# Kernel optimization log

Hardware: AMD Instinct MI355X
Metric: run time of the kernel (lower is better)

## Reference

```python
import jax, jax.numpy as jnp
import numpy as np

N_SRC = 50000
N_DST = 50000
IN_F = 128
OUT_F = 128
N_TYPES = 3
FANOUT = 10
LN_EPS = 1e-12


def setup_inputs() -> dict:
    key = jax.random.key(0)
    ks = jax.random.split(key, 12)
    s_in = 1.0 / np.sqrt(IN_F)
    return {
        "feature": jax.random.normal(ks[0], (N_SRC, IN_F), jnp.float32),
        "neighbor_idx": jax.random.randint(ks[1], (N_TYPES, N_DST, FANOUT), 0, N_SRC),
        "W_ih": jax.random.normal(ks[2], (N_TYPES, 4 * IN_F, IN_F), jnp.float32) * s_in,
        "W_hh": jax.random.normal(ks[3], (N_TYPES, 4 * IN_F, IN_F), jnp.float32) * s_in,
        "b_ih": jax.random.normal(ks[4], (N_TYPES, 4 * IN_F), jnp.float32) * s_in,
        "b_hh": jax.random.normal(ks[5], (N_TYPES, 4 * IN_F), jnp.float32) * s_in,
        "fc_self_w": jax.random.normal(ks[6], (N_TYPES, OUT_F, IN_F), jnp.float32) * s_in,
        "fc_neigh_w": jax.random.normal(ks[7], (N_TYPES, OUT_F, IN_F), jnp.float32) * s_in,
        "sage_bias": jnp.zeros((N_TYPES, OUT_F), jnp.float32),
        "ln_w": jnp.ones((N_TYPES, OUT_F), jnp.float32),
        "ln_b": jnp.zeros((N_TYPES, OUT_F), jnp.float32),
    }


def _lstm_last_hidden(seq, W_ih, W_hh, b_ih, b_hh):
    # seq: [N, F, H_in]; single-layer LSTM, hidden size = input size (DGL SAGEConv lstm reducer).
    N = seq.shape[0]
    H = W_hh.shape[1]
    b = b_ih + b_hh

    def step(carry, x):
        h, c = carry
        gates = x @ W_ih.T + h @ W_hh.T + b  # [N, 4H]
        i, f, g, o = jnp.split(gates, 4, axis=-1)  # torch gate order i,f,g,o
        c = jax.nn.sigmoid(f) * c + jax.nn.sigmoid(i) * jnp.tanh(g)
        h = jax.nn.sigmoid(o) * jnp.tanh(c)
        return (h, c), None

    init = (jnp.zeros((N, H), seq.dtype), jnp.zeros((N, H), seq.dtype))
    (h_n, _), _ = jax.lax.scan(step, init, jnp.swapaxes(seq, 0, 1))
    return h_n  # [N, H]


def _layernorm(x, w, b):
    u = jnp.mean(x, axis=-1, keepdims=True)
    s = jnp.mean((x - u) ** 2, axis=-1, keepdims=True)
    return w * ((x - u) / jnp.sqrt(s + LN_EPS)) + b


def reference(feature, neighbor_idx, W_ih, W_hh, b_ih, b_hh,
              fc_self_w, fc_neigh_w, sage_bias, ln_w, ln_b):
    outs = []
    n_types = neighbor_idx.shape[0]
    for t in range(n_types):
        neigh = feature[neighbor_idx[t]]  # [N_dst, fanout, IN_F] irregular gather
        h_neigh = _lstm_last_hidden(neigh, W_ih[t], W_hh[t], b_ih[t], b_hh[t])
        rst = feature @ fc_self_w[t].T + h_neigh @ fc_neigh_w[t].T + sage_bias[t]
        h = _layernorm(rst, ln_w[t], ln_b[t])
        h = jax.nn.elu(h)  # dropout p=0.0 -> identity
        outs.append(h)
    return jnp.stack(outs, axis=1)  # [N_dst, n_types, OUT_F]
```

## Files before the change

kernel.cpp:

```cpp
#include <hip/hip_runtime.h>
#include <hip/hip_bf16.h>

#define N_SRC_ 50000
#define N_DST_ 50000
#define INF_   128
#define OUTF_  128
#define NT_    3
#define FAN_   10
#define BM_    64

#define LOG2E_  1.4426950408889634f
#define LOG2E2_ 2.8853900817779268f

typedef __attribute__((ext_vector_type(8))) short          bf16x8;
typedef __attribute__((ext_vector_type(4))) float          f32x4;
typedef __attribute__((ext_vector_type(2))) float          f32x2;

__device__ __forceinline__ unsigned short f2bf(float f) {
  unsigned u = __float_as_uint(f);
  u = u + 0x7FFFu + ((u >> 16) & 1u);
  return (unsigned short)(u >> 16);
}
__device__ __forceinline__ float frcp(float x) { return __builtin_amdgcn_rcpf(x); }
__device__ __forceinline__ float fexp2(float x) { return __builtin_amdgcn_exp2f(x); }

__device__ __forceinline__ void gload16(const unsigned short* g, unsigned short* l) {
  __builtin_amdgcn_global_load_lds(
      (const __attribute__((address_space(1))) void*)g,
      (__attribute__((address_space(3))) void*)l, 16, 0, 0);
}

__global__ void prep_feat(const float* __restrict__ f, unsigned short* __restrict__ o, int n4) {
  int i = blockIdx.x * blockDim.x + threadIdx.x;
  if (i < n4) {
    float4 v = ((const float4*)f)[i];
    ushort4 r;
    r.x = f2bf(v.x); r.y = f2bf(v.y); r.z = f2bf(v.z); r.w = f2bf(v.w);
    ((ushort4*)o)[i] = r;
  }
}

__global__ void prep_w(const float* __restrict__ W_ih, const float* __restrict__ W_hh,
                       const float* __restrict__ b_ih, const float* __restrict__ b_hh,
                       const float* __restrict__ fcs,  const float* __restrict__ fcn,
                       unsigned short* __restrict__ Wcat, unsigned short* __restrict__ W2cat,
                       float* __restrict__ bcat) {
  int i = blockIdx.x * blockDim.x + threadIdx.x;
  if (i < NT_ * 512 * 256) {
    int t = i / (512 * 256); int rem = i % (512 * 256);
    int nr = rem >> 8; int kk = rem & 255;
    int w = nr >> 6, ct = (nr >> 4) & 3, j = nr & 15;
    int col = ct * 128 + w * 16 + j;
    float v = (kk < 128) ? W_ih[(t * 512 + col) * 128 + kk]
                         : W_hh[(t * 512 + col) * 128 + (kk - 128)];
    v *= (ct == 2) ? LOG2E2_ : LOG2E_;
    Wcat[i] = f2bf(v);
  } else {
    int i2 = i - NT_ * 512 * 256;
    if (i2 < NT_ * 128 * 256) {
      int t = i2 / (128 * 256); int rem = i2 % (128 * 256);
      int n = rem >> 8; int kk = rem & 255;
      float v = (kk < 128) ? fcs[(t * 128 + n) * 128 + kk]
                           : fcn[(t * 128 + n) * 128 + (kk - 128)];
      W2cat[i2] = f2bf(v);
    } else {
      int i3 = i2 - NT_ * 128 * 256;
      if (i3 < NT_ * 512) {
        int t = i3 / 512; int nr = i3 % 512;
        int ct = (nr >> 4) & 3;
        int col = ct * 128 + (nr >> 6) * 16 + (nr & 15);
        float s = (ct == 2) ? LOG2E2_ : LOG2E_;
        bcat[i3] = (b_ih[t * 512 + col] + b_hh[t * 512 + col]) * s;
      }
    }
  }
}

__global__ __launch_bounds__(512, 2) void sage_main(
    const unsigned short* __restrict__ feat16, const int* __restrict__ nidx,
    const unsigned short* __restrict__ Wcat, const float* __restrict__ bcat,
    const unsigned short* __restrict__ W2cat,
    const float* __restrict__ sbias, const float* __restrict__ lnw,
    const float* __restrict__ lnb, float* __restrict__ out) {
  const int t  = blockIdx.y;
  const int r0 = blockIdx.x * BM_;
  const int tid = threadIdx.x;
  const int w  = tid >> 6;
  const int l  = tid & 63;
  const int lg = l >> 4;
  const int lr = l & 15;

  __shared__ __align__(16) unsigned short lds_x[2][BM_ * INF_];
  __shared__ __align__(16) unsigned short lds_h[2][BM_ * INF_];
  __shared__ int   lds_idx[BM_ * FAN_];
  __shared__ float lds_ps[BM_ * 8];
  __shared__ float lds_pq[BM_ * 8];
  __shared__ float lds_mu[BM_];
  __shared__ float lds_ri[BM_];

  for (int i = tid; i < BM_ * FAN_; i += 512) {
    int row = i / FAN_;
    int v = 0;
    if (r0 + row < N_DST_) v = nidx[(t * N_DST_ + r0) * FAN_ + i];
    v = min(max(v, 0), N_SRC_ - 1);
    lds_idx[i] = v * INF_;
  }

  bf16x8 wfrag[4][8];
  {
    const unsigned short* wb = Wcat + (t * 512 + w * 64) * 256;
#pragma unroll
    for (int ct = 0; ct < 4; ++ct)
#pragma unroll
      for (int kk = 0; kk < 8; ++kk)
        wfrag[ct][kk] = *(const bf16x8*)(wb + (ct * 16 + lr) * 256 + kk * 32 + lg * 8);
  }
  f32x4 biasv[4];
#pragma unroll
  for (int ct = 0; ct < 4; ++ct)
#pragma unroll
    for (int j = 0; j < 4; ++j)
      biasv[ct][j] = bcat[t * 512 + w * 64 + ct * 16 + lg * 4 + j];

  float cst[16];
#pragma unroll
  for (int q = 0; q < 16; ++q) cst[q] = 0.f;

  const int grow = tid >> 4;
  const int gch  = tid & 15;
  const int gsw  = (gch ^ (grow & 7)) * 8;
  const int wb0  = (w * 4) * INF_;
  const int wb1  = (w * 4 + 32) * INF_;
  const int amask = (lr & 7) << 3;
  const int hcw   = w * 2 + (lg >> 1);
  const int hoff  = (lg & 1) << 2;

  __syncthreads();

  {
    int o0 = lds_idx[grow * FAN_];
    int o1 = lds_idx[(grow + 32) * FAN_];
    gload16(feat16 + o0 + gsw, &lds_x[0][wb0]);
    gload16(feat16 + o1 + gsw, &lds_x[0][wb1]);
  }
  __syncthreads();

#pragma unroll 1
  for (int k = 0; k < FAN_; ++k) {
    const int cb = k & 1, nb = cb ^ 1;

    if (k + 1 < FAN_) {
      int o0 = lds_idx[grow * FAN_ + k + 1];
      int o1 = lds_idx[(grow + 32) * FAN_ + k + 1];
      gload16(feat16 + o0 + gsw, &lds_x[nb][wb0]);
      gload16(feat16 + o1 + gsw, &lds_x[nb][wb1]);
    } else {
      int s0 = min(r0 + grow, N_DST_ - 1) * INF_;
      int s1 = min(r0 + grow + 32, N_DST_ - 1) * INF_;
      gload16(feat16 + s0 + gsw, &lds_x[nb][wb0]);
      gload16(feat16 + s1 + gsw, &lds_x[nb][wb1]);
    }

    const unsigned short* xb = lds_x[cb];
    const unsigned short* hb = lds_h[cb];
    unsigned short* hw = lds_h[nb];

    auto mfma_rt = [&](f32x4* acc, int rt) {
#pragma unroll
      for (int ct = 0; ct < 4; ++ct) acc[ct] = biasv[ct];
      __builtin_amdgcn_s_setprio(1);
#pragma unroll
      for (int kk = 0; kk < 8; ++kk) {
        if (kk >= 4 && k == 0) continue;
        const int rowb = (rt * 16 + lr) * INF_;
        bf16x8 b = (kk < 4)
            ? *(const bf16x8*)(xb + rowb + ((kk * 32 + lg * 8) ^ amask))
            : *(const bf16x8*)(hb + rowb + (((kk - 4) * 32 + lg * 8) ^ amask));
#pragma unroll
        for (int ct = 0; ct < 4; ++ct)
          acc[ct] = __builtin_amdgcn_mfma_f32_16x16x32_bf16(wfrag[ct][kk], b, acc[ct], 0, 0, 0);
      }
      __builtin_amdgcn_s_setprio(0);
    };

    auto gates_rt = [&](f32x4* acc, int rt) {
      float hv[4];
#pragma unroll
      for (int jp = 0; jp < 2; ++jp) {
        f32x2 gi = {acc[0][jp * 2], acc[0][jp * 2 + 1]};
        f32x2 gf = {acc[1][jp * 2], acc[1][jp * 2 + 1]};
        f32x2 gg = {acc[2][jp * 2], acc[2][jp * 2 + 1]};
        f32x2 go = {acc[3][jp * 2], acc[3][jp * 2 + 1]};
        f32x2 ei, ef, Eg, eo;
        ei[0] = fexp2(-gi[0]); ei[1] = fexp2(-gi[1]);
        ef[0] = fexp2(-gf[0]); ef[1] = fexp2(-gf[1]);
        Eg[0] = fexp2(gg[0]);  Eg[1] = fexp2(gg[1]);
        eo[0] = fexp2(-go[0]); eo[1] = fexp2(-go[1]);
        f32x2 A = ef + 1.f;
        f32x2 B = ei + 1.f;
        f32x2 E = Eg + 1.f;
        f32x2 F = Eg - 1.f;
        f32x2 cp = {cst[rt * 4 + jp * 2], cst[rt * 4 + jp * 2 + 1]};
        f32x2 BE = B * E;
        f32x2 den = A * BE;
        f32x2 r; r[0] = frcp(den[0]); r[1] = frcp(den[1]);
        f32x2 c2 = (cp * BE + F * A) * r;
        cst[rt * 4 + jp * 2]     = c2[0];
        cst[rt * 4 + jp * 2 + 1] = c2[1];
        f32x2 xc = c2 * LOG2E2_;
        f32x2 Ec; Ec[0] = fexp2(xc[0]); Ec[1] = fexp2(xc[1]);
        f32x2 G = Ec - 1.f;
        f32x2 H = (eo + 1.f) * (Ec + 1.f);
        f32x2 rr; rr[0] = frcp(H[0]); rr[1] = frcp(H[1]);
        f32x2 hvv = G * rr;
        hv[jp * 2] = hvv[0]; hv[jp * 2 + 1] = hvv[1];
      }
      unsigned p01, p23;
      asm("v_cvt_pk_bf16_f32 %0, %1, %2" : "=v"(p01) : "v"(hv[0]), "v"(hv[1]));
      asm("v_cvt_pk_bf16_f32 %0, %1, %2" : "=v"(p23) : "v"(hv[2]), "v"(hv[3]));
      const int row = rt * 16 + lr;
      const int saddr = row * INF_ + (((hcw ^ (row & 7)) << 3) + hoff);
      uint2 pk; pk.x = p01; pk.y = p23;
      *(uint2*)(hw + saddr) = pk;
    };

    f32x4 accA[4], accB[4];
    mfma_rt(accA, 0);
    mfma_rt(accB, 1);
    gates_rt(accA, 0);
    mfma_rt(accA, 2);
    gates_rt(accB, 1);
    mfma_rt(accB, 3);
    gates_rt(accA, 2);
    gates_rt(accB, 3);

    __syncthreads();
  }

  bf16x8 w2f[8];
  {
    const unsigned short* w2b = W2cat + (t * 128 + w * 16) * 256;
#pragma unroll
    for (int kk = 0; kk < 8; ++kk)
      w2f[kk] = *(const bf16x8*)(w2b + lr * 256 + kk * 32 + lg * 8);
  }
  f32x4 b2v, lwv, lbv;
#pragma unroll
  for (int j = 0; j < 4; ++j) {
    b2v[j] = sbias[t * 128 + w * 16 + lg * 4 + j];
    lwv[j] = lnw[t * 128 + w * 16 + lg * 4 + j];
    lbv[j] = lnb[t * 128 + w * 16 + lg * 4 + j];
  }

  f32x4 a2[4];
#pragma unroll
  for (int rt = 0; rt < 4; ++rt) a2[rt] = b2v;
  {
    const unsigned short* xb = lds_x[0];
    const unsigned short* hb = lds_h[0];
    __builtin_amdgcn_s_setprio(1);
#pragma unroll
    for (int kk = 0; kk < 8; ++kk) {
#pragma unroll
      for (int rt = 0; rt < 4; ++rt) {
        const int rowb = (rt * 16 + lr) * INF_;
        bf16x8 b = (kk < 4)
            ? *(const bf16x8*)(xb + rowb + ((kk * 32 + lg * 8) ^ amask))
            : *(const bf16x8*)(hb + rowb + (((kk - 4) * 32 + lg * 8) ^ amask));
        a2[rt] = __builtin_amdgcn_mfma_f32_16x16x32_bf16(w2f[kk], b, a2[rt], 0, 0, 0);
      }
    }
    __builtin_amdgcn_s_setprio(0);
  }

#pragma unroll
  for (int rt = 0; rt < 4; ++rt) {
    float s = a2[rt][0] + a2[rt][1] + a2[rt][2] + a2[rt][3];
    float q = a2[rt][0] * a2[rt][0] + a2[rt][1] * a2[rt][1]
            + a2[rt][2] * a2[rt][2] + a2[rt][3] * a2[rt][3];
    s += __shfl_xor(s, 16, 64); q += __shfl_xor(q, 16, 64);
    s += __shfl_xor(s, 32, 64); q += __shfl_xor(q, 32, 64);
    if (lg == 0) {
      int row = rt * 16 + lr;
      lds_ps[row * 8 + w] = s;
      lds_pq[row * 8 + w] = q;
    }
  }
  __syncthreads();
  if (tid < BM_) {
    float s = 0.f, q = 0.f;
#pragma unroll
    for (int wv = 0; wv < 8; ++wv) { s += lds_ps[tid * 8 + wv]; q += lds_pq[tid * 8 + wv]; }
    float mu = s * (1.f / 128.f);
    float var = q * (1.f / 128.f) - mu * mu;
    lds_mu[tid] = mu;
    lds_ri[tid] = rsqrtf(var + 1e-12f);
  }
  __syncthreads();
#pragma unroll
  for (int rt = 0; rt < 4; ++rt) {
    int row = rt * 16 + lr;
    if (r0 + row < N_DST_) {
      float mu = lds_mu[row], ri = lds_ri[row];
      float4 o;
      float y0 = (a2[rt][0] - mu) * ri * lwv[0] + lbv[0];
      float y1 = (a2[rt][1] - mu) * ri * lwv[1] + lbv[1];
      float y2 = (a2[rt][2] - mu) * ri * lwv[2] + lbv[2];
      float y3 = (a2[rt][3] - mu) * ri * lwv[3] + lbv[3];
      o.x = (y0 > 0.f) ? y0 : (fexp2(y0 * LOG2E_) - 1.f);
      o.y = (y1 > 0.f) ? y1 : (fexp2(y1 * LOG2E_) - 1.f);
      o.z = (y2 > 0.f) ? y2 : (fexp2(y2 * LOG2E_) - 1.f);
      o.w = (y3 > 0.f) ? y3 : (fexp2(y3 * LOG2E_) - 1.f);
      *(float4*)(out + (size_t)(r0 + row) * (NT_ * OUTF_) + t * OUTF_ + w * 16 + lg * 4) = o;
    }
  }
}

extern "C" void kernel_launch(void* const* d_in, const int* in_sizes, int n_in,
                              void* d_out, int out_size, void* d_ws, size_t ws_size,
                              hipStream_t stream) {
  (void)in_sizes; (void)n_in; (void)out_size; (void)ws_size;
  const float* feature = (const float*)d_in[0];
  const int*   nidx    = (const int*)d_in[1];
  const float* W_ih    = (const float*)d_in[2];
  const float* W_hh    = (const float*)d_in[3];
  const float* b_ih    = (const float*)d_in[4];
  const float* b_hh    = (const float*)d_in[5];
  const float* fcs     = (const float*)d_in[6];
  const float* fcn     = (const float*)d_in[7];
  const float* sbias   = (const float*)d_in[8];
  const float* lnw     = (const float*)d_in[9];
  const float* lnb     = (const float*)d_in[10];
  float* out = (float*)d_out;

  char* ws = (char*)d_ws;
  unsigned short* feat16 = (unsigned short*)ws;
  unsigned short* Wcat   = (unsigned short*)(ws + 12800000);
  unsigned short* W2cat  = (unsigned short*)(ws + 12800000 + 786432);
  float*          bcat   = (float*)(ws + 12800000 + 786432 + 196608);

  int n4 = N_SRC_ * INF_ / 4;
  prep_feat<<<(n4 + 255) / 256, 256, 0, stream>>>(feature, feat16, n4);
  int ptot = NT_ * 512 * 256 + NT_ * 128 * 256 + NT_ * 512;
  prep_w<<<(ptot + 255) / 256, 256, 0, stream>>>(W_ih, W_hh, b_ih, b_hh, fcs, fcn, Wcat, W2cat, bcat);

  dim3 grid((N_DST_ + BM_ - 1) / BM_, NT_);
  sage_main<<<grid, 512, 0, stream>>>(feat16, nidx, Wcat, bcat, W2cat, sbias, lnw, lnb, out);
}
```

Measured before the change: 495.4 us.

## Peel first LSTM step and interleave MFMA with gate math via sched_group_barrier

Peels the k=0 LSTM step into its own block that skips the zero-hidden-state MFMAs, and makes the steady-state loop branch-free by selecting the self-feature prefetch address with a conditional. Adds a sched_group_barrier sequence that interleaves MFMA, VALU and DS ops in each step so gate transcendental math overlaps matrix work. Seeds the MFMA accumulators directly from the bias instead of copying it first, and drops the per-step setprio calls. The hand-tuned schedule groups may not match the instructions the compiler actually emits, which could constrain scheduling badly or increase register pressure.

New measurement: 501.3 us. No clear change (+1.2%).

```diff
diff --git a/kernel.cpp b/kernel.cpp
--- a/kernel.cpp
+++ b/kernel.cpp
@@ -28,6 +28,24 @@
   __builtin_amdgcn_global_load_lds(
       (const __attribute__((address_space(1))) void*)g,
       (__attribute__((address_space(3))) void*)l, 16, 0, 0);
+}
+
+__device__ __forceinline__ void sgb_step() {
+  __builtin_amdgcn_sched_group_barrier(0x100, 2, 0);
+  __builtin_amdgcn_sched_group_barrier(0x020, 2, 0);
+  __builtin_amdgcn_sched_group_barrier(0x100, 8, 0);
+#pragma unroll
+  for (int i = 0; i < 24; ++i) {
+    __builtin_amdgcn_sched_group_barrier(0x008, 4, 0);
+    __builtin_amdgcn_sched_group_barrier(0x002, 9, 0);
+    __builtin_amdgcn_sched_group_barrier(0x100, 1, 0);
+  }
+#pragma unroll
+  for (int i = 0; i < 8; ++i) {
+    __builtin_amdgcn_sched_group_barrier(0x008, 4, 0);
+    __builtin_amdgcn_sched_group_barrier(0x002, 9, 0);
+  }
+  __builtin_amdgcn_sched_group_barrier(0x200, 4, 0);
 }
 
 __global__ void prep_feat(const float* __restrict__ f, unsigned short* __restrict__ o, int n4) {
@@ -92,7 +110,7 @@
 
   __shared__ __align__(16) unsigned short lds_x[2][BM_ * INF_];
   __shared__ __align__(16) unsigned short lds_h[2][BM_ * INF_];
-  __shared__ int   lds_idx[BM_ * FAN_];
+  __shared__ int   lds_idx[BM_ * FAN_ + 32];
   __shared__ float lds_ps[BM_ * 8];
   __shared__ float lds_pq[BM_ * 8];
   __shared__ float lds_mu[BM_];
@@ -134,6 +152,8 @@
   const int amask = (lr & 7) << 3;
   const int hcw   = w * 2 + (lg >> 1);
   const int hoff  = (lg & 1) << 2;
+  const int self0 = min(r0 + grow, N_DST_ - 1) * INF_;
+  const int self1 = min(r0 + grow + 32, N_DST_ - 1) * INF_;
 
   __syncthreads();
 
@@ -145,34 +165,107 @@
   }
   __syncthreads();
 
+  auto gates_rt = [&](f32x4* acc, int rt, unsigned short* hw) {
+    float hv[4];
+#pragma unroll
+    for (int jp = 0; jp < 2; ++jp) {
+      f32x2 gi = {acc[0][jp * 2], acc[0][jp * 2 + 1]};
+      f32x2 gf = {acc[1][jp * 2], acc[1][jp * 2 + 1]};
+      f32x2 gg = {acc[2][jp * 2], acc[2][jp * 2 + 1]};
+      f32x2 go = {acc[3][jp * 2], acc[3][jp * 2 + 1]};
+      f32x2 ei, ef, Eg, eo;
+      ei[0] = fexp2(-gi[0]); ei[1] = fexp2(-gi[1]);
+      ef[0] = fexp2(-gf[0]); ef[1] = fexp2(-gf[1]);
+      Eg[0] = fexp2(gg[0]);  Eg[1] = fexp2(gg[1]);
+      eo[0] = fexp2(-go[0]); eo[1] = fexp2(-go[1]);
+      f32x2 A = ef + 1.f;
+      f32x2 B = ei + 1.f;
+      f32x2 E = Eg + 1.f;
+      f32x2 F = Eg - 1.f;
+      f32x2 cp = {cst[rt * 4 + jp * 2], cst[rt * 4 + jp * 2 + 1]};
+      f32x2 BE = B * E;
+      f32x2 den = A * BE;
+      f32x2 r; r[0] = frcp(den[0]); r[1] = frcp(den[1]);
+      f32x2 c2 = (cp * BE + F * A) * r;
+      cst[rt * 4 + jp * 2]     = c2[0];
+      cst[rt * 4 + jp * 2 + 1] = c2[1];
+      f32x2 xc = c2 * LOG2E2_;
+      f32x2 Ec; Ec[0] = fexp2(xc[0]); Ec[1] = fexp2(xc[1]);
+      f32x2 G = Ec - 1.f;
+      f32x2 H = (eo + 1.f) * (Ec + 1.f);
+      f32x2 rr; rr[0] = frcp(H[0]); rr[1] = frcp(H[1]);
+      f32x2 hvv = G * rr;
+      hv[jp * 2] = hvv[0]; hv[jp * 2 + 1] = hvv[1];
+    }
+    unsigned p01, p23;
+    asm("v_cvt_pk_bf16_f32 %0, %1, %2" : "=v"(p01) : "v"(hv[0]), "v"(hv[1]));
+    asm("v_cvt_pk_bf16_f32 %0, %1, %2" : "=v"(p23) : "v"(hv[2]), "v"(hv[3]));
+    const int row = rt * 16 + lr;
+    const int saddr = row * INF_ + (((hcw ^ (row & 7)) << 3) + hoff);
+    uint2 pk; pk.x = p01; pk.y = p23;
+    *(uint2*)(hw + saddr) = pk;
+  };
+
+  {
+    const unsigned short* xb = lds_x[0];
+    unsigned short* hw = lds_h[1];
+    {
+      int o0 = lds_idx[grow * FAN_ + 1];
+      int o1 = lds_idx[(grow + 32) * FAN_ + 1];
+      gload16(feat16 + o0 + gsw, &lds_x[1][wb0]);
+      gload16(feat16 + o1 + gsw, &lds_x[1][wb1]);
+    }
+    auto mfma_x = [&](f32x4* acc, int rt) {
+      const int rowb = (rt * 16 + lr) * INF_;
+      bf16x8 b0 = *(const bf16x8*)(xb + rowb + ((lg * 8) ^ amask));
+#pragma unroll
+      for (int ct = 0; ct < 4; ++ct)
+        acc[ct] = __builtin_amdgcn_mfma_f32_16x16x32_bf16(wfrag[ct][0], b0, biasv[ct], 0, 0, 0);
+#pragma unroll
+      for (int kk = 1; kk < 4; ++kk) {
+        bf16x8 b = *(const bf16x8*)(xb + rowb + ((kk * 32 + lg * 8) ^ amask));
+#pragma unroll
+        for (int ct = 0; ct < 4; ++ct)
+          acc[ct] = __builtin_amdgcn_mfma_f32_16x16x32_bf16(wfrag[ct][kk], b, acc[ct], 0, 0, 0);
+      }
+    };
+    f32x4 accA[4], accB[4];
+    mfma_x(accA, 0);
+    mfma_x(accB, 1);
+    gates_rt(accA, 0, hw);
+    mfma_x(accA, 2);
+    gates_rt(accB, 1, hw);
+    mfma_x(accB, 3);
+    gates_rt(accA, 2, hw);
+    gates_rt(accB, 3, hw);
+    __syncthreads();
+  }
+
 #pragma unroll 1
-  for (int k = 0; k < FAN_; ++k) {
+  for (int k = 1; k < FAN_; ++k) {
     const int cb = k & 1, nb = cb ^ 1;
 
-    if (k + 1 < FAN_) {
+    {
       int o0 = lds_idx[grow * FAN_ + k + 1];
       int o1 = lds_idx[(grow + 32) * FAN_ + k + 1];
+      o0 = (k < FAN_ - 1) ? o0 : self0;
+      o1 = (k < FAN_ - 1) ? o1 : self1;
       gload16(feat16 + o0 + gsw, &lds_x[nb][wb0]);
       gload16(feat16 + o1 + gsw, &lds_x[nb][wb1]);
-    } else {
-      int s0 = min(r0 + grow, N_DST_ - 1) * INF_;
-      int s1 = min(r0 + grow + 32, N_DST_ - 1) * INF_;
-      gload16(feat16 + s0 + gsw, &lds_x[nb][wb0]);
-      gload16(feat16 + s1 + gsw, &lds_x[nb][wb1]);
     }
 
     const unsigned short* xb = lds_x[cb];
     const unsigned short* hb = lds_h[cb];
     unsigned short* hw = lds_h[nb];
 
-    auto mfma_rt = [&](f32x4* acc, int rt) {
-#pragma unroll
-      for (int ct = 0; ct < 4; ++ct) acc[ct] = biasv[ct];
-      __builtin_amdgcn_s_setprio(1);
-#pragma unroll
-      for (int kk = 0; kk < 8; ++kk) {
-        if (kk >= 4 && k == 0) continue;
-        const int rowb = (rt * 16 + lr) * INF_;
+    auto mfma_xh = [&](f32x4* acc, int rt) {
+      const int rowb = (rt * 16 + lr) * INF_;
+      bf16x8 b0 = *(const bf16x8*)(xb + rowb + ((lg * 8) ^ amask));
+#pragma unroll
+      for (int ct = 0; ct < 4; ++ct)
+        acc[ct] = __builtin_amdgcn_mfma_f32_16x16x32_bf16(wfrag[ct][0], b0, biasv[ct], 0, 0, 0);
+#pragma unroll
+      for (int kk = 1; kk < 8; ++kk) {
         bf16x8 b = (kk < 4)
             ? *(const bf16x8*)(xb + rowb + ((kk * 32 + lg * 8) ^ amask))
             : *(const bf16x8*)(hb + rowb + (((kk - 4) * 32 + lg * 8) ^ amask));
@@ -180,59 +273,19 @@
         for (int ct = 0; ct < 4; ++ct)
           acc[ct] = __builtin_amdgcn_mfma_f32_16x16x32_bf16(wfrag[ct][kk], b, acc[ct], 0, 0, 0);
       }
-      __builtin_amdgcn_s_setprio(0);
     };
 
-    auto gates_rt = [&](f32x4* acc, int rt) {
-      float hv[4];
-#pragma unroll
-      for (int jp = 0; jp < 2; ++jp) {
-        f32x2 gi = {acc[0][jp * 2], acc[0][jp * 2 + 1]};
-        f32x2 gf = {acc[1][jp * 2], acc[1][jp * 2 + 1]};
-        f32x2 gg = {acc[2][jp * 2], acc[2][jp * 2 + 1]};
-        f32x2 go = {acc[3][jp * 2], acc[3][jp * 2 + 1]};
-        f32x2 ei, ef, Eg, eo;
-        ei[0] = fexp2(-gi[0]); ei[1] = fexp2(-gi[1]);
-        ef[0] = fexp2(-gf[0]); ef[1] = fexp2(-gf[1]);
-        Eg[0] = fexp2(gg[0]);  Eg[1] = fexp2(gg[1]);
-        eo[0] = fexp2(-go[0]); eo[1] = fexp2(-go[1]);
-        f32x2 A = ef + 1.f;
-        f32x2 B = ei + 1.f;
-        f32x2 E = Eg + 1.f;
-        f32x2 F = Eg - 1.f;
-        f32x2 cp = {cst[rt * 4 + jp * 2], cst[rt * 4 + jp * 2 + 1]};
-        f32x2 BE = B * E;
-        f32x2 den = A * BE;
-        f32x2 r; r[0] = frcp(den[0]); r[1] = frcp(den[1]);
-        f32x2 c2 = (cp * BE + F * A) * r;
-        cst[rt * 4 + jp * 2]     = c2[0];
-        cst[rt * 4 + jp * 2 + 1] = c2[1];
-        f32x2 xc = c2 * LOG2E2_;
-        f32x2 Ec; Ec[0] = fexp2(xc[0]); Ec[1] = fexp2(xc[1]);
-        f32x2 G = Ec - 1.f;
-        f32x2 H = (eo + 1.f) * (Ec + 1.f);
-        f32x2 rr; rr[0] = frcp(H[0]); rr[1] = frcp(H[1]);
-        f32x2 hvv = G * rr;
-        hv[jp * 2] = hvv[0]; hv[jp * 2 + 1] = hvv[1];
-      }
-      unsigned p01, p23;
-      asm("v_cvt_pk_bf16_f32 %0, %1, %2" : "=v"(p01) : "v"(hv[0]), "v"(hv[1]));
-      asm("v_cvt_pk_bf16_f32 %0, %1, %2" : "=v"(p23) : "v"(hv[2]), "v"(hv[3]));
-      const int row = rt * 16 + lr;
-      const int saddr = row * INF_ + (((hcw ^ (row & 7)) << 3) + hoff);
-      uint2 pk; pk.x = p01; pk.y = p23;
-      *(uint2*)(hw + saddr) = pk;
-    };
-
     f32x4 accA[4], accB[4];
-    mfma_rt(accA, 0);
-    mfma_rt(accB, 1);
-    gates_rt(accA, 0);
-    mfma_rt(accA, 2);
-    gates_rt(accB, 1);
-    mfma_rt(accB, 3);
-    gates_rt(accA, 2);
-    gates_rt(accB, 3);
+    mfma_xh(accA, 0);
+    mfma_xh(accB, 1);
+    gates_rt(accA, 0, hw);
+    mfma_xh(accA, 2);
+    gates_rt(accB, 1, hw);
+    mfma_xh(accB, 3);
+    gates_rt(accA, 2, hw);
+    gates_rt(accB, 3, hw);
+
+    sgb_step();
 
     __syncthreads();
   }
@@ -253,14 +306,18 @@
   }
 
   f32x4 a2[4];
-#pragma unroll
-  for (int rt = 0; rt < 4; ++rt) a2[rt] = b2v;
   {
     const unsigned short* xb = lds_x[0];
     const unsigned short* hb = lds_h[0];
     __builtin_amdgcn_s_setprio(1);
 #pragma unroll
-    for (int kk = 0; kk < 8; ++kk) {
+    for (int rt = 0; rt < 4; ++rt) {
+      const int rowb = (rt * 16 + lr) * INF_;
+      bf16x8 b0 = *(const bf16x8*)(xb + rowb + ((lg * 8) ^ amask));
+      a2[rt] = __builtin_amdgcn_mfma_f32_16x16x32_bf16(w2f[0], b0, b2v, 0, 0, 0);
+    }
+#pragma unroll
+    for (int kk = 1; kk < 8; ++kk) {
 #pragma unroll
       for (int rt = 0; rt < 4; ++rt) {
         const int rowb = (rt * 16 + lr) * INF_;
```
